# Performance work log

Measured on AMD Instinct MI355X. Metric: run time of the kernel, lower is better.

Reference implementation:

```python
import jax, jax.numpy as jnp
import numpy as np

G = 512      # graphs per batch
NPG = 64     # nodes per graph (EEG channels)
N = G * NPG  # total nodes = 32768
DEG = 32     # avg degree
E = N * DEG  # total edges = 1048576
F_IN, F1, F2, F3, K = 64, 128, 128, 64, 3


def setup_inputs() -> dict:
    key = jax.random.key(0)
    ks = jax.random.split(key, 8)
    rng = np.random.default_rng(0)
    # block-wise random edges: every edge stays inside its 64-node graph
    base = np.repeat(np.arange(G, dtype=np.int64) * NPG, NPG * DEG)
    row = jnp.asarray(base + rng.integers(0, NPG, E))
    col = jnp.asarray(base + rng.integers(0, NPG, E))
    batch = jnp.asarray(np.repeat(np.arange(G, dtype=np.int64), NPG))
    x = jax.random.normal(ks[0], (N, F_IN), jnp.float32)
    edge_weight = jax.random.uniform(ks[1], (E,), jnp.float32, 0.1, 1.0)

    def xav(k, shape):
        lim = (6.0 / (shape[-2] + shape[-1])) ** 0.5
        return jax.random.uniform(k, shape, jnp.float32, -lim, lim)

    return {
        'x': x, 'edge_weight': edge_weight,
        'W1': xav(ks[2], (K, F_IN, F1)), 'b1': jnp.zeros((F1,), jnp.float32),
        'W2': xav(ks[3], (K, F1, F2)),  'b2': jnp.zeros((F2,), jnp.float32),
        'W3': xav(ks[4], (K, F2, F3)),  'b3': jnp.zeros((F3,), jnp.float32),
        'fc_w': xav(ks[5], (2 * F3, F3)), 'fc_b': jnp.zeros((F3,), jnp.float32),
        'row': row, 'col': col, 'batch': batch,
    }


def cheb_conv(x, row, col, ew, W, b):
    # PyG ChebConv with sym normalization, lambda_max = 2:
    # L_hat = 2L/lambda_max - I = -D^{-1/2} A D^{-1/2}  (diagonal is exactly 0)
    deg = jax.ops.segment_sum(ew, row, num_segments=N)
    safe = jnp.where(deg > 0, deg, 1.0)
    dinv = jnp.where(deg > 0, jax.lax.rsqrt(safe), 0.0)
    nw = -(dinv[row] * ew * dinv[col])  # off-diagonal entries of L_hat

    def prop(t):  # t: [N, F] -> L_hat @ t via gather-scale-scatter
        return jax.ops.segment_sum(nw[:, None] * t[row], col, num_segments=N)

    Tx0 = x
    out = Tx0 @ W[0]
    Tx1 = prop(Tx0)
    out = out + Tx1 @ W[1]
    for k in range(2, K):  # Chebyshev recursion T_k = 2 L_hat T_{k-1} - T_{k-2}
        Tx2 = 2.0 * prop(Tx1) - Tx0
        out = out + Tx2 @ W[k]
        Tx0, Tx1 = Tx1, Tx2
    return out + b


def reference(x, edge_weight, W1, b1, W2, b2, W3, b3, fc_w, fc_b, row, col, batch):
    h = jax.nn.relu(cheb_conv(x, row, col, edge_weight, W1, b1))
    h = jax.nn.relu(cheb_conv(h, row, col, edge_weight, W2, b2))
    h = cheb_conv(h, row, col, edge_weight, W3, b3)
    # meanmax readout over graphs
    counts = jax.ops.segment_sum(jnp.ones((N,), h.dtype), batch, num_segments=G)
    h_mean = jax.ops.segment_sum(h, batch, num_segments=G) / counts[:, None]
    h_max = jax.ops.segment_max(h, batch, num_segments=G)
    pooled = jnp.concatenate([h_mean, h_max], axis=1)  # [G, 2*F3]
    return pooled @ fc_w + fc_b
```

## Files before the change

### kernel.cpp

```cpp
#include <hip/hip_runtime.h>
#include <math.h>

typedef float  f32x4  __attribute__((ext_vector_type(4)));
typedef short  bf16x8 __attribute__((ext_vector_type(8)));

#define NG  512
#define EPG 2048

#define H_OFF    0
#define HT_OFF   16384
#define TN1_OFF  32768
#define TN2_OFF  49152
#define LN_OFF   65536
#define L2N_OFF  73728
#define LDS_SZ   81920

__device__ __forceinline__ unsigned short f2bf(float f) {
    union { float f; unsigned u; } v; v.f = f;
    unsigned r = v.u + 0x7fffu + ((v.u >> 16) & 1u);
    return (unsigned short)(r >> 16);
}
__device__ __forceinline__ bf16x8 ubf(uint4 u) {
    union { uint4 a; bf16x8 b; } c; c.a = u; return c.b;
}

__global__ __launch_bounds__(64) void wpack(
    const float* __restrict__ W1, const float* __restrict__ W2,
    const float* __restrict__ W3, uint4* __restrict__ Wp)
{
    int b = blockIdx.x, lane = threadIdx.x;
    const float* W; int FIN, FOUT, rel, off;
    if (b < 48)       { W = W1; FIN = 64;  FOUT = 128; rel = b;       off = 0;   }
    else if (b < 144) { W = W2; FIN = 128; FOUT = 128; rel = b - 48;  off = 48;  }
    else              { W = W3; FIN = 128; FOUT = 64;  rel = b - 144; off = 144; }
    int NKT = FIN / 32, NNT = FOUT / 16;
    int t3 = rel / (NKT * NNT), r2 = rel % (NKT * NNT);
    int kt = r2 / NNT, nt = r2 % NNT;
    int lg = lane >> 4, li = lane & 15;
    int fin0 = kt*32 + lg*8, fout = nt*16 + li;
    unsigned v[4];
#pragma unroll
    for (int jp = 0; jp < 4; ++jp) {
        unsigned lo = f2bf(W[((size_t)t3*FIN + fin0 + 2*jp    ) * FOUT + fout]);
        unsigned hi = f2bf(W[((size_t)t3*FIN + fin0 + 2*jp + 1) * FOUT + fout]);
        v[jp] = lo | (hi << 16);
    }
    Wp[(size_t)(off + rel)*64 + lane] = make_uint4(v[0],v[1],v[2],v[3]);
}

template <int FIN, int FOUT, bool RELU, bool LAST>
__device__ __forceinline__ void layer(
    char* smem, const uint4* __restrict__ Wp, const float* __restrict__ bias,
    int w, int lg, int li, int lane)
{
    constexpr int NKT = FIN / 32;
    constexpr int NNT = FOUT / 16;
    constexpr int NFO = FOUT / 32;
    constexpr int TST = (FIN == 128) ? 256 : 128;
    constexpr int TSM = (FIN == 128) ? 15 : 7;
    constexpr int NTN = (FIN == 128) ? 4 : 2;

    char* H   = smem + H_OFF;
    char* Ht  = smem + HT_OFF;
    char* Tn1 = smem + TN1_OFF;
    char* Tn2 = smem + TN2_OFF;

    {
        const int mt  = (FIN == 128) ? w : (w & 3);
        const int nt0 = (FIN == 128) ? 0 : ((w >> 2) * 2);
        const int frow = mt*16 + li;
        const int fsw  = (frow & 7) << 4;
        bf16x8 a0[2];
#pragma unroll
        for (int kt = 0; kt < 2; ++kt)
            a0[kt] = *(const bf16x8*)(Ht + frow*128 + ((kt*64 + lg*16) ^ fsw));
#pragma unroll
        for (int j = 0; j < NTN; ++j) {
            const int nt = nt0 + j, nrow = nt*16 + li;
            const int lsw = (nrow & 7) << 4;
            uint4 b1f[2], b2f[2];
#pragma unroll
            for (int kt = 0; kt < 2; ++kt) {
                b1f[kt] = *(const uint4*)(smem + LN_OFF  + nrow*128 + ((kt*64 + lg*16) ^ lsw));
                b2f[kt] = *(const uint4*)(smem + L2N_OFF + nrow*128 + ((kt*64 + lg*16) ^ lsw));
            }
            f32x4 p1 = {0.f,0.f,0.f,0.f}, p2 = {0.f,0.f,0.f,0.f};
            p1 = __builtin_amdgcn_mfma_f32_16x16x32_bf16(a0[0], ubf(b1f[0]), p1, 0,0,0);
            p1 = __builtin_amdgcn_mfma_f32_16x16x32_bf16(a0[1], ubf(b1f[1]), p1, 0,0,0);
            p2 = __builtin_amdgcn_mfma_f32_16x16x32_bf16(a0[0], ubf(b2f[0]), p2, 0,0,0);
            p2 = __builtin_amdgcn_mfma_f32_16x16x32_bf16(a0[1], ubf(b2f[1]), p2, 0,0,0);
            const int cb = ((mt*16 + lg*4)*2) ^ ((nrow & TSM) << 4);
            unsigned short q0 = f2bf(p1[0]), q1 = f2bf(p1[1]), q2 = f2bf(p1[2]), q3 = f2bf(p1[3]);
            *(uint2*)(Tn1 + nrow*TST + cb) =
                make_uint2(q0 | ((unsigned)q1<<16), q2 | ((unsigned)q3<<16));
            q0 = f2bf(p2[0]); q1 = f2bf(p2[1]); q2 = f2bf(p2[2]); q3 = f2bf(p2[3]);
            *(uint2*)(Tn2 + nrow*TST + cb) =
                make_uint2(q0 | ((unsigned)q1<<16), q2 | ((unsigned)q3<<16));
        }
    }
    __syncthreads();

    const int mw = w & 3, foh = w >> 2;
    f32x4 acc[NFO];
#pragma unroll
    for (int f = 0; f < NFO; ++f) acc[f] = (f32x4){0.f,0.f,0.f,0.f};
    {
        const int arow = mw*16 + li;
        const int asw  = (arow & TSM) << 4;
#pragma unroll
        for (int t3 = 0; t3 < 3; ++t3) {
            const char* src = (t3 == 0) ? H : (t3 == 1) ? Tn1 : Tn2;
#pragma unroll
            for (int k = 0; k < NKT; ++k) {
                bf16x8 ta = *(const bf16x8*)(src + arow*TST + ((k*64 + lg*16) ^ asw));
#pragma unroll
                for (int f = 0; f < NFO; ++f) {
                    uint4 wf = Wp[((size_t)(t3*NKT + k)*NNT + foh*NFO + f)*64 + lane];
                    acc[f] = __builtin_amdgcn_mfma_f32_16x16x32_bf16(ta, ubf(wf), acc[f], 0,0,0);
                }
            }
        }
    }
    __syncthreads();

    if (!LAST) {
        constexpr int OST = (FOUT == 128) ? 256 : 128;
        constexpr int OSM = (FOUT == 128) ? 15 : 7;
#pragma unroll
        for (int f = 0; f < NFO; ++f) {
            const int fo = (foh*NFO + f)*16 + li;
            const float bv = bias[fo];
            unsigned short q[4];
#pragma unroll
            for (int r = 0; r < 4; ++r) {
                float o = acc[f][r] + bv;
                if (RELU) o = fmaxf(o, 0.f);
                q[r] = f2bf(o);
            }
            const int node0 = mw*16 + lg*4;
#pragma unroll
            for (int r = 0; r < 4; ++r)
                *(unsigned short*)(H + (node0+r)*OST + ((fo*2) ^ (((node0+r) & OSM) << 4))) = q[r];
            *(uint2*)(Ht + fo*128 + ((node0*2) ^ ((fo & 7) << 4))) =
                make_uint2(q[0] | ((unsigned)q[1]<<16), q[2] | ((unsigned)q[3]<<16));
        }
        __syncthreads();
    } else {
        float* pS = (float*)(smem + LN_OFF);
        float* pM = (float*)(smem + LN_OFF + 1024);
#pragma unroll
        for (int f = 0; f < NFO; ++f) {
            const int fo = (foh*NFO + f)*16 + li;
            f32x4 v = acc[f];
            float s = v[0] + v[1] + v[2] + v[3];
            float m = fmaxf(fmaxf(v[0], v[1]), fmaxf(v[2], v[3]));
            s += __shfl_xor(s, 16); s += __shfl_xor(s, 32);
            m = fmaxf(m, __shfl_xor(m, 16)); m = fmaxf(m, __shfl_xor(m, 32));
            if (lg == 0) { pS[mw*64 + fo] = s; pM[mw*64 + fo] = m; }
        }
        __syncthreads();
    }
}

__global__ __launch_bounds__(512, 4) void fused(
    const float* __restrict__ X,  const float* __restrict__ ew,
    const int* __restrict__ row,  const int* __restrict__ col,
    const uint4* __restrict__ Wp,
    const float* __restrict__ b1, const float* __restrict__ b2,
    const float* __restrict__ b3,
    const float* __restrict__ fcw, const float* __restrict__ fcb,
    float* __restrict__ outp)
{
    __shared__ __align__(16) char smem[LDS_SZ];
    const int g = blockIdx.x, t = threadIdx.x;
    const int w = t >> 6, lane = t & 63, lg = lane >> 4, li = lane & 15;

    const float4* xg = (const float4*)(X + (size_t)g * 4096);
    float4 xv0 = xg[t], xv1 = xg[t + 512];
    const int e0 = g * EPG;
    int er[4], ec[4]; float ev[4];
#pragma unroll
    for (int j = 0; j < 4; ++j) {
        er[j] = row[e0 + t + 512*j] & 63;
        ec[j] = col[e0 + t + 512*j] & 63;
        ev[j] = ew[e0 + t + 512*j];
    }

    float* sA    = (float*)(smem + TN1_OFF);
    float* sdinv = (float*)(smem + TN2_OFF);

    for (int i = t; i < 4096; i += 512) sA[i] = 0.f;
    __syncthreads();
#pragma unroll
    for (int j = 0; j < 4; ++j) atomicAdd(&sA[er[j]*64 + ec[j]], ev[j]);
    __syncthreads();

    {
        const int r = t >> 3, s8 = (t & 7) * 8;
        float p = 0.f;
#pragma unroll
        for (int j = 0; j < 8; ++j) p += sA[r*64 + s8 + j];
        p += __shfl_xor(p, 1); p += __shfl_xor(p, 2); p += __shfl_xor(p, 4);
        if ((t & 7) == 0) sdinv[r] = (p > 0.f) ? rsqrtf(p) : 0.f;
    }
    __syncthreads();

    for (int i = t; i < 4096; i += 512) {
        const int r = i >> 6, c = i & 63;
        sA[i] = -sA[i] * sdinv[r] * sdinv[c];
    }
    __syncthreads();

    {
        const int n = t >> 3, kq = t & 7;
        unsigned vv[4];
#pragma unroll
        for (int jp = 0; jp < 4; ++jp) {
            unsigned lo = f2bf(sA[(kq*8 + 2*jp    )*64 + n]);
            unsigned hi = f2bf(sA[(kq*8 + 2*jp + 1)*64 + n]);
            vv[jp] = lo | (hi << 16);
        }
        *(uint4*)(smem + LN_OFF + n*128 + ((kq*16) ^ ((n & 7) << 4))) =
            make_uint4(vv[0], vv[1], vv[2], vv[3]);
    }
    {
        char* H  = smem + H_OFF;
        char* Ht = smem + HT_OFF;
#pragma unroll
        for (int half = 0; half < 2; ++half) {
            const int i = t + half*512;
            const float4 v = half ? xv1 : xv0;
            const int node = i >> 4, f0 = (i & 15) * 4;
            unsigned short h[4] = { f2bf(v.x), f2bf(v.y), f2bf(v.z), f2bf(v.w) };
            *(uint2*)(H + node*128 + ((f0*2) ^ ((node & 7) << 4))) =
                make_uint2(h[0] | ((unsigned)h[1]<<16), h[2] | ((unsigned)h[3]<<16));
#pragma unroll
            for (int r = 0; r < 4; ++r)
                *(unsigned short*)(Ht + (f0+r)*128 + ((node*2) ^ (((f0+r) & 7) << 4))) = h[r];
        }
    }
    __syncthreads();

    {
        const int mt2 = w & 3, nth = w >> 2;
        const int krow = mt2*16 + li;
        bf16x8 a2[2];
#pragma unroll
        for (int kt = 0; kt < 2; ++kt) {
            const float* sp = &sA[krow*64 + kt*32 + lg*8];
            f32x4 s0 = *(const f32x4*)sp;
            f32x4 s1 = *(const f32x4*)(sp + 4);
            unsigned u0 = f2bf(s0[0]) | ((unsigned)f2bf(s0[1]) << 16);
            unsigned u1 = f2bf(s0[2]) | ((unsigned)f2bf(s0[3]) << 16);
            unsigned u2 = f2bf(s1[0]) | ((unsigned)f2bf(s1[1]) << 16);
            unsigned u3 = f2bf(s1[2]) | ((unsigned)f2bf(s1[3]) << 16);
            a2[kt] = ubf(make_uint4(u0, u1, u2, u3));
        }
#pragma unroll
        for (int j = 0; j < 2; ++j) {
            const int nt = nth*2 + j, nrow = nt*16 + li;
            const int lsw = (nrow & 7) << 4;
            uint4 bf0 = *(const uint4*)(smem + LN_OFF + nrow*128 + ((0*64 + lg*16) ^ lsw));
            uint4 bf1 = *(const uint4*)(smem + LN_OFF + nrow*128 + ((1*64 + lg*16) ^ lsw));
            f32x4 p = {0.f,0.f,0.f,0.f};
            p = __builtin_amdgcn_mfma_f32_16x16x32_bf16(a2[0], ubf(bf0), p, 0,0,0);
            p = __builtin_amdgcn_mfma_f32_16x16x32_bf16(a2[1], ubf(bf1), p, 0,0,0);
            unsigned short q[4];
#pragma unroll
            for (int r = 0; r < 4; ++r) {
                const int k = mt2*16 + lg*4 + r;
                float d = 2.f*p[r] - ((k == nrow) ? 1.f : 0.f);
                q[r] = f2bf(d);
            }
            *(uint2*)(smem + L2N_OFF + nrow*128 + (((mt2*16 + lg*4)*2) ^ lsw)) =
                make_uint2(q[0] | ((unsigned)q[1]<<16), q[2] | ((unsigned)q[3]<<16));
        }
    }
    __syncthreads();

    layer<64, 128, true,  false>(smem, Wp,                  b1, w, lg, li, lane);
    layer<128, 128, true, false>(smem, Wp + (size_t)48*64,  b2, w, lg, li, lane);
    layer<128, 64, false, true >(smem, Wp + (size_t)144*64, b3, w, lg, li, lane);

    float* pS    = (float*)(smem + LN_OFF);
    float* pM    = (float*)(smem + LN_OFF + 1024);
    float* smean = (float*)(smem + L2N_OFF);
    float* smax  = smean + 64;
    float* part  = smax + 64;
    if (t < 64) {
        float s = pS[t] + pS[64+t] + pS[128+t] + pS[192+t];
        float m = fmaxf(fmaxf(pM[t], pM[64+t]), fmaxf(pM[128+t], pM[192+t]));
        smean[t] = s * (1.f/64.f) + b3[t];
        smax[t]  = m + b3[t];
    }
    __syncthreads();
    if (t < 128) {
        const int j = t & 63, h = t >> 6;
        const float* wv = fcw + (size_t)h*64*64;
        const float* sv = h ? smax : smean;
        float a = 0.f;
        for (int f2 = 0; f2 < 64; ++f2) a += sv[f2] * wv[f2*64 + j];
        part[t] = a;
    }
    __syncthreads();
    if (t < 64) outp[(size_t)g*64 + t] = part[t] + part[64 + t] + fcb[t];
}

extern "C" void kernel_launch(void* const* d_in, const int* in_sizes, int n_in,
                              void* d_out, int out_size, void* d_ws, size_t ws_size,
                              hipStream_t stream)
{
    const float* x   = (const float*)d_in[0];
    const float* ew  = (const float*)d_in[1];
    const float* W1  = (const float*)d_in[2];
    const float* b1  = (const float*)d_in[3];
    const float* W2  = (const float*)d_in[4];
    const float* b2  = (const float*)d_in[5];
    const float* W3  = (const float*)d_in[6];
    const float* b3  = (const float*)d_in[7];
    const float* fcw = (const float*)d_in[8];
    const float* fcb = (const float*)d_in[9];
    const int*   row = (const int*)d_in[10];
    const int*   col = (const int*)d_in[11];

    uint4* Wp = (uint4*)d_ws;

    wpack<<<192, 64, 0, stream>>>(W1, W2, W3, Wp);
    fused<<<NG, 512, 0, stream>>>(x, ew, row, col, Wp,
                                  b1, b2, b3, fcw, fcb, (float*)d_out);
}
```

Before: 36.72 us.

## Fold Chebyshev recursion into weight packing and restructure LDS layouts

Rewrites the Chebyshev combination algebraically: the weights are prepacked as W0, W2 and W1-W0, and each layer uses V1=LH+H, V2=L2H and V3=LH as operands, so the separate node-major copy of H is no longer needed. Adds a single feature-partitioned LDS layout for the activations, builds the adjacency transposed with a padded stride and computes degree with atomics, and removes one barrier per layer. It also merges the final FC into a single 64-thread loop. The intent is less LDS traffic, fewer redundant stores and fewer syncs, at the cost of an extra bf16 rounding on the combined terms and a serial FC loop.

```diff
diff --git a/kernel.cpp b/kernel.cpp
--- a/kernel.cpp
+++ b/kernel.cpp
@@ -1,4 +1,5 @@
 #include <hip/hip_runtime.h>
+#include <hip/hip_bf16.h>
 #include <math.h>
 
 typedef float  f32x4  __attribute__((ext_vector_type(4)));
@@ -7,21 +8,31 @@
 #define NG  512
 #define EPG 2048
 
-#define H_OFF    0
-#define HT_OFF   16384
-#define TN1_OFF  32768
-#define TN2_OFF  49152
-#define LN_OFF   65536
-#define L2N_OFF  73728
-#define LDS_SZ   81920
-
-__device__ __forceinline__ unsigned short f2bf(float f) {
-    union { float f; unsigned u; } v; v.f = f;
-    unsigned r = v.u + 0x7fffu + ((v.u >> 16) & 1u);
-    return (unsigned short)(r >> 16);
-}
-__device__ __forceinline__ bf16x8 ubf(uint4 u) {
+#define B1_OFF 0
+#define B2_OFF 16384
+#define B3_OFF 32768
+#define B4_OFF 49152
+#define B5_OFF 65536
+#define LDS_SZ 81920
+#define SASTR  65
+
+static __device__ __forceinline__ unsigned short f2bf(float f) {
+    union { __hip_bfloat16 b; unsigned short u; } c;
+    c.b = __float2bfloat16(f);
+    return c.u;
+}
+static __device__ __forceinline__ float bf2f(unsigned short h) {
+    union { unsigned u; float f; } v; v.u = ((unsigned)h) << 16;
+    return v.f;
+}
+static __device__ __forceinline__ unsigned pk2(float lo, float hi) {
+    return (unsigned)f2bf(lo) | ((unsigned)f2bf(hi) << 16);
+}
+static __device__ __forceinline__ bf16x8 ubf(uint4 u) {
     union { uint4 a; bf16x8 b; } c; c.a = u; return c.b;
+}
+static __device__ __forceinline__ int fpart(int f) {
+    return ((((f >> 5) << 1) + ((f >> 2) & 1)) << 9) + (((f >> 3) & 3) << 7) + ((f & 3) << 5);
 }
 
 __global__ __launch_bounds__(64) void wpack(
@@ -34,68 +45,82 @@
     else if (b < 144) { W = W2; FIN = 128; FOUT = 128; rel = b - 48;  off = 48;  }
     else              { W = W3; FIN = 128; FOUT = 64;  rel = b - 144; off = 144; }
     int NKT = FIN / 32, NNT = FOUT / 16;
-    int t3 = rel / (NKT * NNT), r2 = rel % (NKT * NNT);
+    int sl = rel / (NKT * NNT), r2 = rel % (NKT * NNT);
     int kt = r2 / NNT, nt = r2 % NNT;
     int lg = lane >> 4, li = lane & 15;
     int fin0 = kt*32 + lg*8, fout = nt*16 + li;
     unsigned v[4];
 #pragma unroll
     for (int jp = 0; jp < 4; ++jp) {
-        unsigned lo = f2bf(W[((size_t)t3*FIN + fin0 + 2*jp    ) * FOUT + fout]);
-        unsigned hi = f2bf(W[((size_t)t3*FIN + fin0 + 2*jp + 1) * FOUT + fout]);
-        v[jp] = lo | (hi << 16);
+        float a0, a1;
+#pragma unroll
+        for (int h = 0; h < 2; ++h) {
+            const size_t base = (size_t)(fin0 + 2*jp + h) * FOUT + fout;
+            const float w0 = W[base];
+            const float w1v = W[(size_t)FIN*FOUT + base];
+            const float w2v = W[(size_t)2*FIN*FOUT + base];
+            const float val = (sl == 0) ? w0 : (sl == 1) ? w2v : (w1v - w0);
+            if (h == 0) a0 = val; else a1 = val;
+        }
+        v[jp] = pk2(a0, a1);
     }
     Wp[(size_t)(off + rel)*64 + lane] = make_uint4(v[0],v[1],v[2],v[3]);
 }
 
 template <int FIN, int FOUT, bool RELU, bool LAST>
-__device__ __forceinline__ void layer(
+static __device__ __forceinline__ void layer(
     char* smem, const uint4* __restrict__ Wp, const float* __restrict__ bias,
     int w, int lg, int li, int lane)
 {
     constexpr int NKT = FIN / 32;
     constexpr int NNT = FOUT / 16;
     constexpr int NFO = FOUT / 32;
-    constexpr int TST = (FIN == 128) ? 256 : 128;
+    constexpr int TST = FIN * 2;
     constexpr int TSM = (FIN == 128) ? 15 : 7;
-    constexpr int NTN = (FIN == 128) ? 4 : 2;
-
-    char* H   = smem + H_OFF;
-    char* Ht  = smem + HT_OFF;
-    char* Tn1 = smem + TN1_OFF;
-    char* Tn2 = smem + TN2_OFF;
+    constexpr int NGS = (FIN >> 4) * 512;
+
+    char* Hio = smem + B1_OFF;
+    char* V1  = smem + B2_OFF;
+    char* V2  = smem + B3_OFF;
+    char* V3  = smem + B4_OFF;
+    const char* Ln  = smem + B5_OFF;
+    const char* L2n = smem + B5_OFF + 8192;
 
     {
         const int mt  = (FIN == 128) ? w : (w & 3);
         const int nt0 = (FIN == 128) ? 0 : ((w >> 2) * 2);
-        const int frow = mt*16 + li;
-        const int fsw  = (frow & 7) << 4;
-        bf16x8 a0[2];
+        constexpr int NTN = (FIN == 128) ? 4 : 2;
+        const int f  = mt * 16 + li;
+        const int fp = fpart(f) + ((lg & 1) << 4);
+        bf16x8 a[2];
 #pragma unroll
         for (int kt = 0; kt < 2; ++kt)
-            a0[kt] = *(const bf16x8*)(Ht + frow*128 + ((kt*64 + lg*16) ^ fsw));
+            a[kt] = *(const bf16x8*)(Hio + (kt * 2 + (lg >> 1)) * NGS + fp);
+        const int fb    = mt * 16 + lg * 4;
+        const int fpb   = fpart(fb);
+        const int fcol2 = fb * 2;
 #pragma unroll
         for (int j = 0; j < NTN; ++j) {
-            const int nt = nt0 + j, nrow = nt*16 + li;
-            const int lsw = (nrow & 7) << 4;
-            uint4 b1f[2], b2f[2];
+            const int nrow = (nt0 + j) * 16 + li;
+            const int lsw  = (nrow & 7) << 4;
+            f32x4 p2 = {0.f,0.f,0.f,0.f}, p3 = {0.f,0.f,0.f,0.f};
 #pragma unroll
             for (int kt = 0; kt < 2; ++kt) {
-                b1f[kt] = *(const uint4*)(smem + LN_OFF  + nrow*128 + ((kt*64 + lg*16) ^ lsw));
-                b2f[kt] = *(const uint4*)(smem + L2N_OFF + nrow*128 + ((kt*64 + lg*16) ^ lsw));
+                uint4 bL  = *(const uint4*)(Ln  + nrow*128 + ((kt*64 + lg*16) ^ lsw));
+                uint4 bL2 = *(const uint4*)(L2n + nrow*128 + ((kt*64 + lg*16) ^ lsw));
+                p3 = __builtin_amdgcn_mfma_f32_16x16x32_bf16(a[kt], ubf(bL),  p3, 0,0,0);
+                p2 = __builtin_amdgcn_mfma_f32_16x16x32_bf16(a[kt], ubf(bL2), p2, 0,0,0);
             }
-            f32x4 p1 = {0.f,0.f,0.f,0.f}, p2 = {0.f,0.f,0.f,0.f};
-            p1 = __builtin_amdgcn_mfma_f32_16x16x32_bf16(a0[0], ubf(b1f[0]), p1, 0,0,0);
-            p1 = __builtin_amdgcn_mfma_f32_16x16x32_bf16(a0[1], ubf(b1f[1]), p1, 0,0,0);
-            p2 = __builtin_amdgcn_mfma_f32_16x16x32_bf16(a0[0], ubf(b2f[0]), p2, 0,0,0);
-            p2 = __builtin_amdgcn_mfma_f32_16x16x32_bf16(a0[1], ubf(b2f[1]), p2, 0,0,0);
-            const int cb = ((mt*16 + lg*4)*2) ^ ((nrow & TSM) << 4);
-            unsigned short q0 = f2bf(p1[0]), q1 = f2bf(p1[1]), q2 = f2bf(p1[2]), q3 = f2bf(p1[3]);
-            *(uint2*)(Tn1 + nrow*TST + cb) =
-                make_uint2(q0 | ((unsigned)q1<<16), q2 | ((unsigned)q3<<16));
-            q0 = f2bf(p2[0]); q1 = f2bf(p2[1]); q2 = f2bf(p2[2]); q3 = f2bf(p2[3]);
-            *(uint2*)(Tn2 + nrow*TST + cb) =
-                make_uint2(q0 | ((unsigned)q1<<16), q2 | ((unsigned)q3<<16));
+            const char* t0p = Hio + (nt0 + j) * NGS + fpb + li * 2;
+            float t0v[4];
+#pragma unroll
+            for (int r = 0; r < 4; ++r)
+                t0v[r] = bf2f(*(const unsigned short*)(t0p + r * 32));
+            const int cb = fcol2 ^ ((nrow & TSM) << 4);
+            *(uint2*)(V1 + nrow*TST + cb) =
+                make_uint2(pk2(p3[0]+t0v[0], p3[1]+t0v[1]), pk2(p3[2]+t0v[2], p3[3]+t0v[3]));
+            *(uint2*)(V2 + nrow*TST + cb) = make_uint2(pk2(p2[0],p2[1]), pk2(p2[2],p2[3]));
+            *(uint2*)(V3 + nrow*TST + cb) = make_uint2(pk2(p3[0],p3[1]), pk2(p3[2],p3[3]));
         }
     }
     __syncthreads();
@@ -103,63 +128,51 @@
     const int mw = w & 3, foh = w >> 2;
     f32x4 acc[NFO];
 #pragma unroll
-    for (int f = 0; f < NFO; ++f) acc[f] = (f32x4){0.f,0.f,0.f,0.f};
+    for (int i = 0; i < NFO; ++i) acc[i] = (f32x4){0.f,0.f,0.f,0.f};
     {
-        const int arow = mw*16 + li;
+        const int arow = mw * 16 + li;
         const int asw  = (arow & TSM) << 4;
 #pragma unroll
-        for (int t3 = 0; t3 < 3; ++t3) {
-            const char* src = (t3 == 0) ? H : (t3 == 1) ? Tn1 : Tn2;
+        for (int sl = 0; sl < 3; ++sl) {
+            const char* src = (sl == 0) ? V1 : (sl == 1) ? V2 : V3;
 #pragma unroll
             for (int k = 0; k < NKT; ++k) {
                 bf16x8 ta = *(const bf16x8*)(src + arow*TST + ((k*64 + lg*16) ^ asw));
 #pragma unroll
-                for (int f = 0; f < NFO; ++f) {
-                    uint4 wf = Wp[((size_t)(t3*NKT + k)*NNT + foh*NFO + f)*64 + lane];
-                    acc[f] = __builtin_amdgcn_mfma_f32_16x16x32_bf16(ta, ubf(wf), acc[f], 0,0,0);
+                for (int fi = 0; fi < NFO; ++fi) {
+                    uint4 wf = Wp[((size_t)(sl*NKT + k)*NNT + foh*NFO + fi)*64 + lane];
+                    acc[fi] = __builtin_amdgcn_mfma_f32_16x16x32_bf16(ta, ubf(wf), acc[fi], 0,0,0);
                 }
             }
         }
     }
-    __syncthreads();
-
     if (!LAST) {
-        constexpr int OST = (FOUT == 128) ? 256 : 128;
-        constexpr int OSM = (FOUT == 128) ? 15 : 7;
-#pragma unroll
-        for (int f = 0; f < NFO; ++f) {
-            const int fo = (foh*NFO + f)*16 + li;
+        constexpr int OGS = (FOUT >> 4) * 512;
+#pragma unroll
+        for (int fi = 0; fi < NFO; ++fi) {
+            const int fo = (foh*NFO + fi)*16 + li;
             const float bv = bias[fo];
-            unsigned short q[4];
-#pragma unroll
-            for (int r = 0; r < 4; ++r) {
-                float o = acc[f][r] + bv;
-                if (RELU) o = fmaxf(o, 0.f);
-                q[r] = f2bf(o);
-            }
-            const int node0 = mw*16 + lg*4;
-#pragma unroll
-            for (int r = 0; r < 4; ++r)
-                *(unsigned short*)(H + (node0+r)*OST + ((fo*2) ^ (((node0+r) & OSM) << 4))) = q[r];
-            *(uint2*)(Ht + fo*128 + ((node0*2) ^ ((fo & 7) << 4))) =
-                make_uint2(q[0] | ((unsigned)q[1]<<16), q[2] | ((unsigned)q[3]<<16));
-        }
-        __syncthreads();
+            f32x4 v = acc[fi];
+            float o0 = v[0]+bv, o1 = v[1]+bv, o2 = v[2]+bv, o3 = v[3]+bv;
+            if (RELU) { o0=fmaxf(o0,0.f); o1=fmaxf(o1,0.f); o2=fmaxf(o2,0.f); o3=fmaxf(o3,0.f); }
+            *(uint2*)(Hio + mw*OGS + fpart(fo) + lg*8) =
+                make_uint2(pk2(o0,o1), pk2(o2,o3));
+        }
     } else {
-        float* pS = (float*)(smem + LN_OFF);
-        float* pM = (float*)(smem + LN_OFF + 1024);
-#pragma unroll
-        for (int f = 0; f < NFO; ++f) {
-            const int fo = (foh*NFO + f)*16 + li;
-            f32x4 v = acc[f];
-            float s = v[0] + v[1] + v[2] + v[3];
-            float m = fmaxf(fmaxf(v[0], v[1]), fmaxf(v[2], v[3]));
+        float* pS = (float*)(smem + B5_OFF + 8192);
+        float* pM = pS + 256;
+#pragma unroll
+        for (int fi = 0; fi < NFO; ++fi) {
+            const int fo = (foh*NFO + fi)*16 + li;
+            f32x4 v = acc[fi];
+            float s = v[0]+v[1]+v[2]+v[3];
+            float m = fmaxf(fmaxf(v[0],v[1]), fmaxf(v[2],v[3]));
             s += __shfl_xor(s, 16); s += __shfl_xor(s, 32);
             m = fmaxf(m, __shfl_xor(m, 16)); m = fmaxf(m, __shfl_xor(m, 32));
             if (lg == 0) { pS[mw*64 + fo] = s; pM[mw*64 + fo] = m; }
         }
-        __syncthreads();
-    }
+    }
+    __syncthreads();
 }
 
 __global__ __launch_bounds__(512, 4) void fused(
@@ -186,94 +199,79 @@
         ev[j] = ew[e0 + t + 512*j];
     }
 
-    float* sA    = (float*)(smem + TN1_OFF);
-    float* sdinv = (float*)(smem + TN2_OFF);
-
-    for (int i = t; i < 4096; i += 512) sA[i] = 0.f;
-    __syncthreads();
-#pragma unroll
-    for (int j = 0; j < 4; ++j) atomicAdd(&sA[er[j]*64 + ec[j]], ev[j]);
-    __syncthreads();
-
+    float* sAT  = (float*)(smem + B2_OFF);
+    float* sdeg = (float*)(smem + B4_OFF);
+
+    for (int i = t; i < 64 * SASTR; i += 512) sAT[i] = 0.f;
+    if (t < 64) sdeg[t] = 0.f;
+    __syncthreads();
+#pragma unroll
+    for (int j = 0; j < 4; ++j) {
+        atomicAdd(&sAT[ec[j]*SASTR + er[j]], ev[j]);
+        atomicAdd(&sdeg[er[j]], ev[j]);
+    }
+    __syncthreads();
     {
-        const int r = t >> 3, s8 = (t & 7) * 8;
-        float p = 0.f;
-#pragma unroll
-        for (int j = 0; j < 8; ++j) p += sA[r*64 + s8 + j];
-        p += __shfl_xor(p, 1); p += __shfl_xor(p, 2); p += __shfl_xor(p, 4);
-        if ((t & 7) == 0) sdinv[r] = (p > 0.f) ? rsqrtf(p) : 0.f;
-    }
-    __syncthreads();
-
-    for (int i = t; i < 4096; i += 512) {
-        const int r = i >> 6, c = i & 63;
-        sA[i] = -sA[i] * sdinv[r] * sdinv[c];
-    }
-    __syncthreads();
-
-    {
-        const int n = t >> 3, kq = t & 7;
-        unsigned vv[4];
-#pragma unroll
-        for (int jp = 0; jp < 4; ++jp) {
-            unsigned lo = f2bf(sA[(kq*8 + 2*jp    )*64 + n]);
-            unsigned hi = f2bf(sA[(kq*8 + 2*jp + 1)*64 + n]);
-            vv[jp] = lo | (hi << 16);
-        }
-        *(uint4*)(smem + LN_OFF + n*128 + ((kq*16) ^ ((n & 7) << 4))) =
-            make_uint4(vv[0], vv[1], vv[2], vv[3]);
-    }
-    {
-        char* H  = smem + H_OFF;
-        char* Ht = smem + HT_OFF;
+        const int n = t >> 3, k0 = (t & 7) * 8;
+        const float dsn = sdeg[n];
+        const float dn = dsn > 0.f ? rsqrtf(dsn) : 0.f;
+        float vv[8];
+#pragma unroll
+        for (int j = 0; j < 8; ++j) {
+            const float dk0 = sdeg[k0 + j];
+            const float dk = dk0 > 0.f ? rsqrtf(dk0) : 0.f;
+            const float v = -sAT[n*SASTR + k0 + j] * dk * dn;
+            sAT[n*SASTR + k0 + j] = v;
+            vv[j] = v;
+        }
+        *(uint4*)(smem + B5_OFF + n*128 + ((k0*2) ^ ((n & 7) << 4))) =
+            make_uint4(pk2(vv[0],vv[1]), pk2(vv[2],vv[3]), pk2(vv[4],vv[5]), pk2(vv[6],vv[7]));
 #pragma unroll
         for (int half = 0; half < 2; ++half) {
-            const int i = t + half*512;
+            const int i = t + half * 512;
             const float4 v = half ? xv1 : xv0;
             const int node = i >> 4, f0 = (i & 15) * 4;
-            unsigned short h[4] = { f2bf(v.x), f2bf(v.y), f2bf(v.z), f2bf(v.w) };
-            *(uint2*)(H + node*128 + ((f0*2) ^ ((node & 7) << 4))) =
-                make_uint2(h[0] | ((unsigned)h[1]<<16), h[2] | ((unsigned)h[3]<<16));
-#pragma unroll
-            for (int r = 0; r < 4; ++r)
-                *(unsigned short*)(Ht + (f0+r)*128 + ((node*2) ^ (((f0+r) & 7) << 4))) = h[r];
-        }
-    }
-    __syncthreads();
-
+            char* base = smem + B1_OFF + ((node >> 4) * 2048) + ((node & 15) << 1);
+            *(unsigned short*)(base + fpart(f0 + 0)) = f2bf(v.x);
+            *(unsigned short*)(base + fpart(f0 + 1)) = f2bf(v.y);
+            *(unsigned short*)(base + fpart(f0 + 2)) = f2bf(v.z);
+            *(unsigned short*)(base + fpart(f0 + 3)) = f2bf(v.w);
+        }
+    }
+    __syncthreads();
     {
         const int mt2 = w & 3, nth = w >> 2;
-        const int krow = mt2*16 + li;
+        const int k1 = mt2*16 + li;
         bf16x8 a2[2];
 #pragma unroll
         for (int kt = 0; kt < 2; ++kt) {
-            const float* sp = &sA[krow*64 + kt*32 + lg*8];
-            f32x4 s0 = *(const f32x4*)sp;
-            f32x4 s1 = *(const f32x4*)(sp + 4);
-            unsigned u0 = f2bf(s0[0]) | ((unsigned)f2bf(s0[1]) << 16);
-            unsigned u1 = f2bf(s0[2]) | ((unsigned)f2bf(s0[3]) << 16);
-            unsigned u2 = f2bf(s1[0]) | ((unsigned)f2bf(s1[1]) << 16);
-            unsigned u3 = f2bf(s1[2]) | ((unsigned)f2bf(s1[3]) << 16);
-            a2[kt] = ubf(make_uint4(u0, u1, u2, u3));
+            float av[8];
+#pragma unroll
+            for (int j = 0; j < 8; ++j)
+                av[j] = sAT[(kt*32 + lg*8 + j)*SASTR + k1];
+            union { uint4 u; bf16x8 b; } c;
+            c.u = make_uint4(pk2(av[0],av[1]), pk2(av[2],av[3]),
+                             pk2(av[4],av[5]), pk2(av[6],av[7]));
+            a2[kt] = c.b;
         }
 #pragma unroll
         for (int j = 0; j < 2; ++j) {
-            const int nt = nth*2 + j, nrow = nt*16 + li;
-            const int lsw = (nrow & 7) << 4;
-            uint4 bf0 = *(const uint4*)(smem + LN_OFF + nrow*128 + ((0*64 + lg*16) ^ lsw));
-            uint4 bf1 = *(const uint4*)(smem + LN_OFF + nrow*128 + ((1*64 + lg*16) ^ lsw));
+            const int nrow = (nth*2 + j)*16 + li;
+            const int lsw  = (nrow & 7) << 4;
             f32x4 p = {0.f,0.f,0.f,0.f};
-            p = __builtin_amdgcn_mfma_f32_16x16x32_bf16(a2[0], ubf(bf0), p, 0,0,0);
-            p = __builtin_amdgcn_mfma_f32_16x16x32_bf16(a2[1], ubf(bf1), p, 0,0,0);
+#pragma unroll
+            for (int kt = 0; kt < 2; ++kt) {
+                uint4 bf = *(const uint4*)(smem + B5_OFF + nrow*128 + ((kt*64 + lg*16) ^ lsw));
+                p = __builtin_amdgcn_mfma_f32_16x16x32_bf16(a2[kt], ubf(bf), p, 0,0,0);
+            }
             unsigned short q[4];
 #pragma unroll
             for (int r = 0; r < 4; ++r) {
-                const int k = mt2*16 + lg*4 + r;
-                float d = 2.f*p[r] - ((k == nrow) ? 1.f : 0.f);
-                q[r] = f2bf(d);
+                const int kk = mt2*16 + lg*4 + r;
+                q[r] = f2bf(2.f*p[r] - ((kk == nrow) ? 1.f : 0.f));
             }
-            *(uint2*)(smem + L2N_OFF + nrow*128 + (((mt2*16 + lg*4)*2) ^ lsw)) =
-                make_uint2(q[0] | ((unsigned)q[1]<<16), q[2] | ((unsigned)q[3]<<16));
+            *(uint2*)(smem + B5_OFF + 8192 + nrow*128 + (((mt2*16 + lg*4)*2) ^ lsw)) =
+                make_uint2(q[0] | ((unsigned)q[1] << 16), q[2] | ((unsigned)q[3] << 16));
         }
     }
     __syncthreads();
@@ -282,28 +280,23 @@
     layer<128, 128, true, false>(smem, Wp + (size_t)48*64,  b2, w, lg, li, lane);
     layer<128, 64, false, true >(smem, Wp + (size_t)144*64, b3, w, lg, li, lane);
 
-    float* pS    = (float*)(smem + LN_OFF);
-    float* pM    = (float*)(smem + LN_OFF + 1024);
-    float* smean = (float*)(smem + L2N_OFF);
-    float* smax  = smean + 64;
-    float* part  = smax + 64;
+    float* pS  = (float*)(smem + B5_OFF + 8192);
+    float* pM  = pS + 256;
+    float* sme = (float*)(smem + B3_OFF);
+    float* smx = sme + 64;
     if (t < 64) {
         float s = pS[t] + pS[64+t] + pS[128+t] + pS[192+t];
         float m = fmaxf(fmaxf(pM[t], pM[64+t]), fmaxf(pM[128+t], pM[192+t]));
-        smean[t] = s * (1.f/64.f) + b3[t];
-        smax[t]  = m + b3[t];
-    }
-    __syncthreads();
-    if (t < 128) {
-        const int j = t & 63, h = t >> 6;
-        const float* wv = fcw + (size_t)h*64*64;
-        const float* sv = h ? smax : smean;
-        float a = 0.f;
-        for (int f2 = 0; f2 < 64; ++f2) a += sv[f2] * wv[f2*64 + j];
-        part[t] = a;
-    }
-    __syncthreads();
-    if (t < 64) outp[(size_t)g*64 + t] = part[t] + part[64 + t] + fcb[t];
+        sme[t] = s * (1.f/64.f) + b3[t];
+        smx[t] = m + b3[t];
+    }
+    __syncthreads();
+    if (t < 64) {
+        float a = fcb[t];
+        for (int f2 = 0; f2 < 64; ++f2)
+            a += sme[f2]*fcw[f2*64 + t] + smx[f2]*fcw[(64 + f2)*64 + t];
+        outp[(size_t)g*64 + t] = a;
+    }
 }
 
 extern "C" void kernel_launch(void* const* d_in, const int* in_sizes, int n_in,
```

After: 41.90 us. +14.1%, slower.
